# Optimization experiments

Measured on AMD Instinct MI355X. Metric: run time of the kernel, lower is better.

Reference implementation:

```python
import jax, jax.numpy as jnp
import numpy as np

HEADS = 4
OUT_CH = 16
NEG_SLOPE = 0.2


def setup_inputs() -> dict:
    key = jax.random.key(0)
    k1, k2, k3, k4 = jax.random.split(key, 4)
    N, E, IN = 50000, 800000, 128
    x = jax.random.normal(k1, (N, IN), dtype=jnp.float32)
    edge_index = jax.random.randint(k2, (2, E), 0, N, dtype=jnp.int32)
    weight = jax.random.normal(k3, (IN, HEADS * OUT_CH), dtype=jnp.float32) * 0.1
    att = jax.random.normal(k4, (1, HEADS, 2 * OUT_CH), dtype=jnp.float32) * 0.1
    bias = jnp.zeros((HEADS * OUT_CH,), dtype=jnp.float32)
    return {"x": x, "edge_index": edge_index, "weight": weight, "att": att, "bias": bias}


def reference(x, edge_index, weight, att, bias):
    N = x.shape[0]
    # add self loops
    loops = jnp.broadcast_to(jnp.arange(N, dtype=edge_index.dtype)[None, :], (2, N))
    ei = jnp.concatenate([edge_index, loops], axis=1)  # [2, E+N]
    h = (x @ weight).reshape(N, HEADS, OUT_CH)  # [N, H, C]
    row, col = ei[0], ei[1]
    x_i = h[row]  # [E', H, C]
    x_j = h[col]  # [E', H, C]
    att_i = att[:, :, :OUT_CH]  # [1, H, C]
    att_j = att[:, :, OUT_CH:]
    alpha = (x_i * att_i).sum(-1) + (x_j * att_j).sum(-1)  # [E', H]
    alpha = jax.nn.leaky_relu(alpha, NEG_SLOPE)
    # NOTE: faithful to the source, softmax over the heads dim (dim=1)
    alpha = jax.nn.softmax(alpha, axis=1)
    out = jnp.zeros((N, HEADS, OUT_CH), dtype=x.dtype)
    out = out.at[col].add(x_i * alpha[..., None])  # scatter-add over destination col
    out = out.reshape(N, HEADS * OUT_CH) + bias
    return out
```

## Files before the change

### kernel.cpp

```cpp
#include <hip/hip_runtime.h>

#define HEADS 4
#define OUT_CH 16
#define CCH 64
#define IN_CH 128
#define NEG_SLOPE 0.2f
#define CAP 48
#define CAPB 5120
#define TILE_A 2048
#define BSTRIDE 32

typedef unsigned int       uint32;
typedef unsigned short     u16;
typedef __attribute__((ext_vector_type(8))) short short8;
typedef __attribute__((ext_vector_type(4))) float f32x4;

__device__ __forceinline__ uint32 bf16_rne(float f) {
    uint32 u = __float_as_uint(f);
    return (u + 0x7fffu + ((u >> 16) & 1u)) >> 16;
}

__global__ __launch_bounds__(256) void k_pre(int* __restrict__ cur, int N,
                                             const float* __restrict__ x,
                                             const float* __restrict__ w,
                                             const float* __restrict__ att,
                                             u16* __restrict__ wTg,
                                             int* __restrict__ bcur, int NBUK,
                                             float* __restrict__ d_i,
                                             float* __restrict__ d_j,
                                             int ZB) {
    int t = threadIdx.x;
    int b = blockIdx.x;

    if (b < ZB) {
        int i = b * 256 + t;
        if (i < N) cur[i] = 0;
        return;
    }
    if (b == ZB) {
        int c = t & 63, half = t >> 6;
        #pragma unroll
        for (int kk = 0; kk < 32; ++kk) {
            int k = half * 32 + kk;
            wTg[c * 128 + k] = (u16)bf16_rne(w[k * CCH + c]);
        }
        for (int i = t; i < NBUK * BSTRIDE; i += 256) bcur[i] = 0;
        return;
    }

    __shared__ float wXf[8][132];
    for (int idx = t; idx < 1024; idx += 256) {
        int k = idx >> 3, j = idx & 7, h = j & 3;
        const float* ab = att + h * (2 * OUT_CH) + ((j >= 4) ? OUT_CH : 0);
        float s = 0.f;
        #pragma unroll
        for (int c = 0; c < 16; ++c)
            s = fmaf(w[k * CCH + h * OUT_CH + c], ab[c], s);
        wXf[j][k] = s;
    }
    __syncthreads();

    int r = (b - ZB - 1) * 32 + (t >> 3);
    int j = t & 7;
    if (r >= N) return;
    const float4* x4 = (const float4*)(x + (size_t)r * IN_CH);
    float s0 = 0.f, s1 = 0.f, s2 = 0.f, s3 = 0.f;
    #pragma unroll
    for (int k4 = 0; k4 < 32; ++k4) {
        float4 v = x4[k4];
        s0 = fmaf(v.x, wXf[j][k4 * 4 + 0], s0);
        s1 = fmaf(v.y, wXf[j][k4 * 4 + 1], s1);
        s2 = fmaf(v.z, wXf[j][k4 * 4 + 2], s2);
        s3 = fmaf(v.w, wXf[j][k4 * 4 + 3], s3);
    }
    float d = (s0 + s1) + (s2 + s3);
    if (j < 4) d_i[r * HEADS + j] = d;
    else       d_j[r * HEADS + (j - 4)] = d;
}

__global__ __launch_bounds__(256) void k_fat(const float* __restrict__ x,
                                             const u16* __restrict__ wTg,
                                             u16* __restrict__ h_bf,
                                             const int* __restrict__ rows,
                                             const int* __restrict__ cols,
                                             int* __restrict__ bcur,
                                             uint32* __restrict__ bucketbuf,
                                             int N, int E, int GB, int NBUK) {
    int t = threadIdx.x;

    if ((int)blockIdx.x < GB) {
        int lane = t & 63;
        int col = lane & 15, g = (lane >> 4) * 8;
        int tile = blockIdx.x * 4 + (t >> 6);
        int ntiles = (N + 15) >> 4;
        if (tile >= ntiles) return;

        int r0 = tile * 16 + (lane & 15);
        if (r0 >= N) r0 = N - 1;
        const float* xp = x + (size_t)r0 * IN_CH + g;
        float4 cu[8];
        #pragma unroll
        for (int kc = 0; kc < 4; ++kc) {
            cu[kc * 2]     = *(const float4*)(xp + kc * 32);
            cu[kc * 2 + 1] = *(const float4*)(xp + kc * 32 + 4);
        }

        short8 bfrag[4][4];
        #pragma unroll
        for (int nt = 0; nt < 4; ++nt)
            #pragma unroll
            for (int kc = 0; kc < 4; ++kc)
                bfrag[nt][kc] = *(const short8*)&wTg[(nt * 16 + col) * 128 + kc * 32 + g];

        short8 af[4];
        #pragma unroll
        for (int kc = 0; kc < 4; ++kc) {
            float4 u = cu[kc * 2], v = cu[kc * 2 + 1];
            short8 s;
            s[0] = (short)bf16_rne(u.x); s[1] = (short)bf16_rne(u.y);
            s[2] = (short)bf16_rne(u.z); s[3] = (short)bf16_rne(u.w);
            s[4] = (short)bf16_rne(v.x); s[5] = (short)bf16_rne(v.y);
            s[6] = (short)bf16_rne(v.z); s[7] = (short)bf16_rne(v.w);
            af[kc] = s;
        }

        f32x4 acc[4] = {{0.f,0.f,0.f,0.f},{0.f,0.f,0.f,0.f},
                        {0.f,0.f,0.f,0.f},{0.f,0.f,0.f,0.f}};
        #pragma unroll
        for (int kc = 0; kc < 4; ++kc)
            #pragma unroll
            for (int nt = 0; nt < 4; ++nt)
                acc[nt] = __builtin_amdgcn_mfma_f32_16x16x32_bf16(
                    af[kc], bfrag[nt][kc], acc[nt], 0, 0, 0);

        int rb = tile * 16;
        #pragma unroll
        for (int nt = 0; nt < 4; ++nt)
            #pragma unroll
            for (int r = 0; r < 4; ++r) {
                int row = rb + (lane >> 4) * 4 + r;
                if (row < N)
                    h_bf[(size_t)row * CCH + nt * 16 + col] =
                        (u16)bf16_rne(acc[nt][r]);
            }
    } else {
        __shared__ int lcnt[256];
        __shared__ int lofs[256];
        __shared__ int lbase[256];
        __shared__ int wsum[4];
        __shared__ uint32 recbuf[TILE_A];
        __shared__ int    gbuf[TILE_A];
        int b = (int)blockIdx.x - GB;
        int e0 = b * TILE_A;
        int tot = E + N;
        int lane = t & 63, wid = t >> 6;

        lcnt[t] = 0;
        __syncthreads();

        int mybkt[8], myrank[8];
        uint32 myrec[8];
        #pragma unroll
        for (int i = 0; i < 8; ++i) {
            int e = e0 + i * 256 + t;
            if (e < tot) {
                int c = (e < E) ? cols[e] : (e - E);
                int r = (e < E) ? rows[e] : c;
                int bk = c >> 8;
                mybkt[i] = bk;
                myrec[i] = (uint32)r | ((uint32)(c & 255) << 17);
                myrank[i] = atomicAdd(&lcnt[bk], 1);
            } else {
                mybkt[i] = -1;
            }
        }
        __syncthreads();

        int v = lcnt[t];
        int sc = v;
        #pragma unroll
        for (int off = 1; off < 64; off <<= 1) {
            int u = __shfl_up(sc, off);
            if (lane >= off) sc += u;
        }
        if (lane == 63) wsum[wid] = sc;
        __syncthreads();
        int wb = 0;
        for (int j = 0; j < wid; ++j) wb += wsum[j];
        lofs[t] = wb + sc - v;
        if (t < NBUK && v > 0)
            lbase[t] = atomicAdd(&bcur[t * BSTRIDE], v);
        __syncthreads();

        #pragma unroll
        for (int i = 0; i < 8; ++i) {
            if (mybkt[i] < 0) continue;
            int bk = mybkt[i];
            int slot = lofs[bk] + myrank[i];
            int bpos = lbase[bk] + myrank[i];
            recbuf[slot] = myrec[i];
            gbuf[slot] = (bpos < CAPB) ? (bk * CAPB + bpos) : -1;
        }
        __syncthreads();

        int nrec = tot - e0;
        if (nrec > TILE_A) nrec = TILE_A;
        for (int sidx = t; sidx < nrec; sidx += 256) {
            int gp = gbuf[sidx];
            if (gp >= 0) bucketbuf[gp] = recbuf[sidx];
        }
    }
}

__global__ __launch_bounds__(256) void k_bucket(const int* __restrict__ bcur,
                                                const uint32* __restrict__ bucketbuf,
                                                uint32* __restrict__ srec,
                                                int* __restrict__ cur, int N) {
    __shared__ uint32 win[256 * CAP];
    __shared__ int lcur[256];
    int t = threadIdx.x;
    int b = blockIdx.x;

    lcur[t] = 0;
    __syncthreads();

    int cnt = bcur[b * BSTRIDE];
    if (cnt > CAPB) cnt = CAPB;
    const uint32* bb = bucketbuf + (size_t)b * CAPB;
    for (int i = t; i < cnt; i += 256) {
        uint32 rec = bb[i];
        int crel = (rec >> 17) & 255;
        int pos = atomicAdd(&lcur[crel], 1);
        if (pos < CAP)
            win[crel * CAP + pos] = rec & 0x1FFFFu;
    }
    __syncthreads();

    int c0 = b << 8;
    int nd = N - c0;
    if (nd > 256) nd = 256;
    int nent = nd * CAP;
    uint32* dst = srec + (size_t)c0 * CAP;
    for (int i = t; i < nent; i += 256) dst[i] = win[i];
    if (t < nd) {
        int v = lcur[t];
        cur[c0 + t] = (v > CAP) ? CAP : v;
    }
}

__global__ __launch_bounds__(256) void k_accum(const int* __restrict__ cur,
                                               const uint32* __restrict__ srec,
                                               const u16* __restrict__ h_bf,
                                               const float* __restrict__ d_i,
                                               const float* __restrict__ d_j,
                                               const float* __restrict__ bias,
                                               float* __restrict__ out, int N) {
    int t = threadIdx.x;
    int wid = t >> 6, lane = t & 63;
    int g = lane >> 4, sub = lane & 15;
    int node = blockIdx.x * 16 + wid * 4 + g;
    int c = (node < N) ? node : N - 1;

    int dg = cur[c];
    if (dg > CAP) dg = CAP;
    int s = c * CAP;
    int md = dg;
    md = max(md, __shfl_xor(md, 16));
    md = max(md, __shfl_xor(md, 32));

    float4 dj4 = *(const float4*)(d_j + (size_t)c * HEADS);
    int hsel = sub >> 2;
    float a0 = 0.f, a1 = 0.f, a2 = 0.f, a3 = 0.f;

    #pragma unroll 4
    for (int r = 0; r < md; ++r) {
        int idx = s + ((r < dg) ? r : (dg - 1));
        int row = (int)srec[idx];
        float4 di4 = *(const float4*)(d_i + (size_t)row * HEADS);
        float l0 = di4.x + dj4.x, l1 = di4.y + dj4.y;
        float l2 = di4.z + dj4.z, l3 = di4.w + dj4.w;
        l0 = l0 > 0.f ? l0 : NEG_SLOPE * l0;
        l1 = l1 > 0.f ? l1 : NEG_SLOPE * l1;
        l2 = l2 > 0.f ? l2 : NEG_SLOPE * l2;
        l3 = l3 > 0.f ? l3 : NEG_SLOPE * l3;
        float m = fmaxf(fmaxf(l0, l1), fmaxf(l2, l3));
        float e0 = __expf(l0 - m), e1 = __expf(l1 - m);
        float e2 = __expf(l2 - m), e3 = __expf(l3 - m);
        float inv = 1.f / (e0 + e1 + e2 + e3);
        float eh = (hsel < 2) ? (hsel == 0 ? e0 : e1) : (hsel == 2 ? e2 : e3);
        float a = eh * inv;
        if (r >= dg) a = 0.f;
        uint2 hb = *(const uint2*)(h_bf + (size_t)row * CCH + sub * 4);
        a0 = fmaf(__uint_as_float(hb.x << 16),           a, a0);
        a1 = fmaf(__uint_as_float(hb.x & 0xffff0000u),   a, a1);
        a2 = fmaf(__uint_as_float(hb.y << 16),           a, a2);
        a3 = fmaf(__uint_as_float(hb.y & 0xffff0000u),   a, a3);
    }

    if (node < N) {
        float4 b = *(const float4*)(bias + sub * 4);
        float4 o = {a0 + b.x, a1 + b.y, a2 + b.z, a3 + b.w};
        *(float4*)(out + (size_t)node * CCH + sub * 4) = o;
    }
}

extern "C" void kernel_launch(void* const* d_in, const int* in_sizes, int n_in,
                              void* d_out, int out_size, void* d_ws, size_t ws_size,
                              hipStream_t stream) {
    const float* x    = (const float*)d_in[0];
    const int*   ei   = (const int*)  d_in[1];
    const float* w    = (const float*)d_in[2];
    const float* att  = (const float*)d_in[3];
    const float* bias = (const float*)d_in[4];
    float* out = (float*)d_out;

    int N = in_sizes[0] / IN_CH;
    int E = in_sizes[1] / 2;
    const int* rows = ei;
    const int* cols = ei + E;
    int total_e = E + N;
    int NBUK = (N + 255) >> 8;

    char* ws = (char*)d_ws;
    auto carve = [&](size_t bytes) {
        char* p = ws;
        ws += (bytes + 255) & ~(size_t)255;
        return p;
    };
    u16*    h_bf      = (u16*)   carve((size_t)N * CCH * 2);
    float*  di        = (float*) carve((size_t)N * HEADS * 4);
    float*  dj        = (float*) carve((size_t)N * HEADS * 4);
    int*    cur       = (int*)   carve((size_t)N * 4);
    int*    bcur      = (int*)   carve((size_t)NBUK * BSTRIDE * 4);
    uint32* srec      = (uint32*)carve((size_t)N * CAP * 4);
    u16*    wTg       = (u16*)   carve((size_t)64 * 128 * 2);
    uint32* bucketbuf = (uint32*)carve((size_t)NBUK * CAPB * 4);

    int ntiles = (N + 15) >> 4;
    int GB = (ntiles + 3) / 4;
    int AB = (total_e + TILE_A - 1) / TILE_A;
    int ZB = (N + 255) / 256;
    int DB = (N + 31) / 32;

    k_pre<<<ZB + 1 + DB, 256, 0, stream>>>(cur, N, x, w, att, wTg, bcur, NBUK,
                                           di, dj, ZB);
    k_fat<<<GB + AB, 256, 0, stream>>>(x, wTg, h_bf, rows, cols,
                                       bcur, bucketbuf, N, E, GB, NBUK);
    k_bucket<<<NBUK, 256, 0, stream>>>(bcur, bucketbuf, srec, cur, N);
    k_accum<<<(N + 15) / 16, 256, 0, stream>>>(cur, srec, h_bf, di, dj, bias, out, N);
}
```

Before: 97.97 us.

## Fuse attention logits into MFMA GEMM, precompute quantized softmax weights in bucketing

Computes the per-node attention logits d_i/d_j as an extra MFMA tile in the projection kernel, which removes the separate fp32 pass over x in k_pre. Softmax weights are now computed once per edge in k_bucket and packed as 11-bit quantized values next to the row index in 64-bit records. The accumulation is split into two launches, each over half of the channels, so each pass gathers a smaller h slice, and it uses nontemporal loads and stores. The cost is twice as much record storage and reading the records twice. The 11-bit weights and bf16 logit weights also reduce accuracy.

Measured after the change: 100.2 us. 1.02x slower.

```diff
diff --git a/kernel.cpp b/kernel.cpp
--- a/kernel.cpp
+++ b/kernel.cpp
@@ -11,76 +11,51 @@
 #define BSTRIDE 32
 
 typedef unsigned int       uint32;
+typedef unsigned long long u64;
 typedef unsigned short     u16;
 typedef __attribute__((ext_vector_type(8))) short short8;
 typedef __attribute__((ext_vector_type(4))) float f32x4;
+typedef __attribute__((ext_vector_type(2))) float f32x2;
 
 __device__ __forceinline__ uint32 bf16_rne(float f) {
     uint32 u = __float_as_uint(f);
     return (u + 0x7fffu + ((u >> 16) & 1u)) >> 16;
 }
 
-__global__ __launch_bounds__(256) void k_pre(int* __restrict__ cur, int N,
-                                             const float* __restrict__ x,
-                                             const float* __restrict__ w,
+__global__ __launch_bounds__(256) void k_pre(const float* __restrict__ w,
                                              const float* __restrict__ att,
                                              u16* __restrict__ wTg,
-                                             int* __restrict__ bcur, int NBUK,
+                                             u16* __restrict__ wXg,
+                                             int* __restrict__ bcur, int NBUK) {
+    int t = threadIdx.x;
+    int c = t & 63, half = t >> 6;
+    #pragma unroll
+    for (int kk = 0; kk < 32; ++kk) {
+        int k = half * 32 + kk;
+        wTg[c * 128 + k] = (u16)bf16_rne(w[k * CCH + c]);
+    }
+    int j = t & 7, h = j & 3, kb = t >> 3;
+    const float* ab = att + h * (2 * OUT_CH) + ((j >= 4) ? OUT_CH : 0);
+    #pragma unroll
+    for (int kk = 0; kk < 4; ++kk) {
+        int k = kb * 4 + kk;
+        float s = 0.f;
+        #pragma unroll
+        for (int cc = 0; cc < 16; ++cc)
+            s = fmaf(w[k * CCH + h * OUT_CH + cc], ab[cc], s);
+        wXg[j * 128 + k] = (u16)bf16_rne(s);
+    }
+    for (int i = t; i < 8 * 128; i += 256) wXg[8 * 128 + i] = 0;
+    for (int i = t; i < NBUK * BSTRIDE; i += 256) bcur[i] = 0;
+}
+
+__global__ __launch_bounds__(256) void k_fat(const float* __restrict__ x,
+                                             const u16* __restrict__ wTg,
+                                             const u16* __restrict__ wXg,
+                                             u16* __restrict__ h0,
+                                             u16* __restrict__ h1,
                                              float* __restrict__ d_i,
                                              float* __restrict__ d_j,
-                                             int ZB) {
-    int t = threadIdx.x;
-    int b = blockIdx.x;
-
-    if (b < ZB) {
-        int i = b * 256 + t;
-        if (i < N) cur[i] = 0;
-        return;
-    }
-    if (b == ZB) {
-        int c = t & 63, half = t >> 6;
-        #pragma unroll
-        for (int kk = 0; kk < 32; ++kk) {
-            int k = half * 32 + kk;
-            wTg[c * 128 + k] = (u16)bf16_rne(w[k * CCH + c]);
-        }
-        for (int i = t; i < NBUK * BSTRIDE; i += 256) bcur[i] = 0;
-        return;
-    }
-
-    __shared__ float wXf[8][132];
-    for (int idx = t; idx < 1024; idx += 256) {
-        int k = idx >> 3, j = idx & 7, h = j & 3;
-        const float* ab = att + h * (2 * OUT_CH) + ((j >= 4) ? OUT_CH : 0);
-        float s = 0.f;
-        #pragma unroll
-        for (int c = 0; c < 16; ++c)
-            s = fmaf(w[k * CCH + h * OUT_CH + c], ab[c], s);
-        wXf[j][k] = s;
-    }
-    __syncthreads();
-
-    int r = (b - ZB - 1) * 32 + (t >> 3);
-    int j = t & 7;
-    if (r >= N) return;
-    const float4* x4 = (const float4*)(x + (size_t)r * IN_CH);
-    float s0 = 0.f, s1 = 0.f, s2 = 0.f, s3 = 0.f;
-    #pragma unroll
-    for (int k4 = 0; k4 < 32; ++k4) {
-        float4 v = x4[k4];
-        s0 = fmaf(v.x, wXf[j][k4 * 4 + 0], s0);
-        s1 = fmaf(v.y, wXf[j][k4 * 4 + 1], s1);
-        s2 = fmaf(v.z, wXf[j][k4 * 4 + 2], s2);
-        s3 = fmaf(v.w, wXf[j][k4 * 4 + 3], s3);
-    }
-    float d = (s0 + s1) + (s2 + s3);
-    if (j < 4) d_i[r * HEADS + j] = d;
-    else       d_j[r * HEADS + (j - 4)] = d;
-}
-
-__global__ __launch_bounds__(256) void k_fat(const float* __restrict__ x,
-                                             const u16* __restrict__ wTg,
-                                             u16* __restrict__ h_bf,
                                              const int* __restrict__ rows,
                                              const int* __restrict__ cols,
                                              int* __restrict__ bcur,
@@ -105,12 +80,15 @@
             cu[kc * 2 + 1] = *(const float4*)(xp + kc * 32 + 4);
         }
 
-        short8 bfrag[4][4];
+        short8 bfrag[4][4], bfrag5[4];
         #pragma unroll
         for (int nt = 0; nt < 4; ++nt)
             #pragma unroll
             for (int kc = 0; kc < 4; ++kc)
                 bfrag[nt][kc] = *(const short8*)&wTg[(nt * 16 + col) * 128 + kc * 32 + g];
+        #pragma unroll
+        for (int kc = 0; kc < 4; ++kc)
+            bfrag5[kc] = *(const short8*)&wXg[col * 128 + kc * 32 + g];
 
         short8 af[4];
         #pragma unroll
@@ -126,23 +104,39 @@
 
         f32x4 acc[4] = {{0.f,0.f,0.f,0.f},{0.f,0.f,0.f,0.f},
                         {0.f,0.f,0.f,0.f},{0.f,0.f,0.f,0.f}};
-        #pragma unroll
-        for (int kc = 0; kc < 4; ++kc)
+        f32x4 accX = {0.f, 0.f, 0.f, 0.f};
+        #pragma unroll
+        for (int kc = 0; kc < 4; ++kc) {
             #pragma unroll
             for (int nt = 0; nt < 4; ++nt)
                 acc[nt] = __builtin_amdgcn_mfma_f32_16x16x32_bf16(
                     af[kc], bfrag[nt][kc], acc[nt], 0, 0, 0);
+            accX = __builtin_amdgcn_mfma_f32_16x16x32_bf16(
+                af[kc], bfrag5[kc], accX, 0, 0, 0);
+        }
 
         int rb = tile * 16;
         #pragma unroll
-        for (int nt = 0; nt < 4; ++nt)
+        for (int nt = 0; nt < 4; ++nt) {
+            u16* hp = (nt < 2) ? h0 : h1;
+            int cc = (nt & 1) * 16 + col;
             #pragma unroll
             for (int r = 0; r < 4; ++r) {
                 int row = rb + (lane >> 4) * 4 + r;
                 if (row < N)
-                    h_bf[(size_t)row * CCH + nt * 16 + col] =
-                        (u16)bf16_rne(acc[nt][r]);
+                    hp[(size_t)row * 32 + cc] = (u16)bf16_rne(acc[nt][r]);
             }
+        }
+        if (col < 8) {
+            #pragma unroll
+            for (int r = 0; r < 4; ++r) {
+                int row = rb + (lane >> 4) * 4 + r;
+                if (row < N) {
+                    if (col < 4) d_i[row * HEADS + col] = accX[r];
+                    else         d_j[row * HEADS + (col - 4)] = accX[r];
+                }
+            }
+        }
     } else {
         __shared__ int lcnt[256];
         __shared__ int lofs[256];
@@ -214,14 +208,21 @@
 
 __global__ __launch_bounds__(256) void k_bucket(const int* __restrict__ bcur,
                                                 const uint32* __restrict__ bucketbuf,
-                                                uint32* __restrict__ srec,
+                                                const float* __restrict__ d_i,
+                                                const float* __restrict__ d_j,
+                                                u64* __restrict__ srec,
                                                 int* __restrict__ cur, int N) {
-    __shared__ uint32 win[256 * CAP];
+    __shared__ u64 win[256 * CAP];
     __shared__ int lcur[256];
+    __shared__ float4 djl[256];
     int t = threadIdx.x;
     int b = blockIdx.x;
+    int c0 = b << 8;
 
     lcur[t] = 0;
+    int cidx = c0 + t;
+    djl[t] = (cidx < N) ? *(const float4*)(d_j + (size_t)cidx * HEADS)
+                        : make_float4(0.f, 0.f, 0.f, 0.f);
     __syncthreads();
 
     int cnt = bcur[b * BSTRIDE];
@@ -229,54 +230,10 @@
     const uint32* bb = bucketbuf + (size_t)b * CAPB;
     for (int i = t; i < cnt; i += 256) {
         uint32 rec = bb[i];
+        int row  = rec & 0x1FFFF;
         int crel = (rec >> 17) & 255;
-        int pos = atomicAdd(&lcur[crel], 1);
-        if (pos < CAP)
-            win[crel * CAP + pos] = rec & 0x1FFFFu;
-    }
-    __syncthreads();
-
-    int c0 = b << 8;
-    int nd = N - c0;
-    if (nd > 256) nd = 256;
-    int nent = nd * CAP;
-    uint32* dst = srec + (size_t)c0 * CAP;
-    for (int i = t; i < nent; i += 256) dst[i] = win[i];
-    if (t < nd) {
-        int v = lcur[t];
-        cur[c0 + t] = (v > CAP) ? CAP : v;
-    }
-}
-
-__global__ __launch_bounds__(256) void k_accum(const int* __restrict__ cur,
-                                               const uint32* __restrict__ srec,
-                                               const u16* __restrict__ h_bf,
-                                               const float* __restrict__ d_i,
-                                               const float* __restrict__ d_j,
-                                               const float* __restrict__ bias,
-                                               float* __restrict__ out, int N) {
-    int t = threadIdx.x;
-    int wid = t >> 6, lane = t & 63;
-    int g = lane >> 4, sub = lane & 15;
-    int node = blockIdx.x * 16 + wid * 4 + g;
-    int c = (node < N) ? node : N - 1;
-
-    int dg = cur[c];
-    if (dg > CAP) dg = CAP;
-    int s = c * CAP;
-    int md = dg;
-    md = max(md, __shfl_xor(md, 16));
-    md = max(md, __shfl_xor(md, 32));
-
-    float4 dj4 = *(const float4*)(d_j + (size_t)c * HEADS);
-    int hsel = sub >> 2;
-    float a0 = 0.f, a1 = 0.f, a2 = 0.f, a3 = 0.f;
-
-    #pragma unroll 4
-    for (int r = 0; r < md; ++r) {
-        int idx = s + ((r < dg) ? r : (dg - 1));
-        int row = (int)srec[idx];
         float4 di4 = *(const float4*)(d_i + (size_t)row * HEADS);
+        float4 dj4 = djl[crel];
         float l0 = di4.x + dj4.x, l1 = di4.y + dj4.y;
         float l2 = di4.z + dj4.z, l3 = di4.w + dj4.w;
         l0 = l0 > 0.f ? l0 : NEG_SLOPE * l0;
@@ -287,20 +244,70 @@
         float e0 = __expf(l0 - m), e1 = __expf(l1 - m);
         float e2 = __expf(l2 - m), e3 = __expf(l3 - m);
         float inv = 1.f / (e0 + e1 + e2 + e3);
-        float eh = (hsel < 2) ? (hsel == 0 ? e0 : e1) : (hsel == 2 ? e2 : e3);
-        float a = eh * inv;
+        uint32 q0 = (uint32)(e0 * inv * 2047.f + 0.5f);
+        uint32 q1 = (uint32)(e1 * inv * 2047.f + 0.5f);
+        uint32 q2 = (uint32)(e2 * inv * 2047.f + 0.5f);
+        uint32 q3 = (uint32)(e3 * inv * 2047.f + 0.5f);
+        u64 prec = (u64)(uint32)row
+                 | ((u64)q0 << 17) | ((u64)q1 << 28)
+                 | ((u64)q2 << 39) | ((u64)q3 << 50);
+        int pos = atomicAdd(&lcur[crel], 1);
+        if (pos < CAP)
+            win[crel * CAP + pos] = prec;
+    }
+    __syncthreads();
+
+    int nd = N - c0;
+    if (nd > 256) nd = 256;
+    int nent = nd * CAP;
+    u64* dst = srec + (size_t)c0 * CAP;
+    for (int i = t; i < nent; i += 256) dst[i] = win[i];
+    if (t < nd) {
+        int v = lcur[t];
+        cur[c0 + t] = (v > CAP) ? CAP : v;
+    }
+}
+
+__global__ __launch_bounds__(256) void k_accum(const int* __restrict__ cur,
+                                               const u64* __restrict__ srec,
+                                               const u16* __restrict__ hp,
+                                               const float* __restrict__ bias,
+                                               float* __restrict__ out,
+                                               int N, int half) {
+    int t = threadIdx.x;
+    int wid = t >> 6, lane = t & 63;
+    int g = lane >> 4, sub = lane & 15;
+    int node = blockIdx.x * 16 + wid * 4 + g;
+    int c = (node < N) ? node : N - 1;
+
+    int dg = cur[c];
+    if (dg > CAP) dg = CAP;
+    size_t s = (size_t)c * CAP;
+    int md = dg;
+    md = max(md, __shfl_xor(md, 16));
+    md = max(md, __shfl_xor(md, 32));
+
+    int ch0 = half * 32 + sub * 2;
+    int shift = 17 + 11 * (ch0 >> 4);
+    float a0 = 0.f, a1 = 0.f;
+
+    #pragma unroll 8
+    for (int r = 0; r < md; ++r) {
+        size_t idx = s + ((r < dg) ? r : (dg - 1));
+        u64 rec = __builtin_nontemporal_load(srec + idx);
+        int row = (int)((uint32)rec & 0x1FFFFu);
+        float a = (float)((uint32)(rec >> shift) & 0x7FFu) * (1.f / 2047.f);
         if (r >= dg) a = 0.f;
-        uint2 hb = *(const uint2*)(h_bf + (size_t)row * CCH + sub * 4);
-        a0 = fmaf(__uint_as_float(hb.x << 16),           a, a0);
-        a1 = fmaf(__uint_as_float(hb.x & 0xffff0000u),   a, a1);
-        a2 = fmaf(__uint_as_float(hb.y << 16),           a, a2);
-        a3 = fmaf(__uint_as_float(hb.y & 0xffff0000u),   a, a3);
+        uint32 hb = *(const uint32*)(hp + (size_t)row * 32 + sub * 2);
+        a0 = fmaf(__uint_as_float(hb << 16),         a, a0);
+        a1 = fmaf(__uint_as_float(hb & 0xffff0000u), a, a1);
     }
 
     if (node < N) {
-        float4 b = *(const float4*)(bias + sub * 4);
-        float4 o = {a0 + b.x, a1 + b.y, a2 + b.z, a3 + b.w};
-        *(float4*)(out + (size_t)node * CCH + sub * 4) = o;
+        f32x2 o;
+        o.x = a0 + bias[ch0];
+        o.y = a1 + bias[ch0 + 1];
+        __builtin_nontemporal_store(o, (f32x2*)(out + (size_t)node * CCH + ch0));
     }
 }
 
@@ -327,25 +334,26 @@
         ws += (bytes + 255) & ~(size_t)255;
         return p;
     };
-    u16*    h_bf      = (u16*)   carve((size_t)N * CCH * 2);
+    u16*    h0        = (u16*)   carve((size_t)N * 32 * 2);
+    u16*    h1        = (u16*)   carve((size_t)N * 32 * 2);
     float*  di        = (float*) carve((size_t)N * HEADS * 4);
     float*  dj        = (float*) carve((size_t)N * HEADS * 4);
     int*    cur       = (int*)   carve((size_t)N * 4);
     int*    bcur      = (int*)   carve((size_t)NBUK * BSTRIDE * 4);
-    uint32* srec      = (uint32*)carve((size_t)N * CAP * 4);
+    u64*    srec      = (u64*)   carve((size_t)N * CAP * 8);
     u16*    wTg       = (u16*)   carve((size_t)64 * 128 * 2);
+    u16*    wXg       = (u16*)   carve((size_t)16 * 128 * 2);
     uint32* bucketbuf = (uint32*)carve((size_t)NBUK * CAPB * 4);
 
     int ntiles = (N + 15) >> 4;
     int GB = (ntiles + 3) / 4;
     int AB = (total_e + TILE_A - 1) / TILE_A;
-    int ZB = (N + 255) / 256;
-    int DB = (N + 31) / 32;
-
-    k_pre<<<ZB + 1 + DB, 256, 0, stream>>>(cur, N, x, w, att, wTg, bcur, NBUK,
-                                           di, dj, ZB);
-    k_fat<<<GB + AB, 256, 0, stream>>>(x, wTg, h_bf, rows, cols,
+    int NACC = (N + 15) / 16;
+
+    k_pre<<<1, 256, 0, stream>>>(w, att, wTg, wXg, bcur, NBUK);
+    k_fat<<<GB + AB, 256, 0, stream>>>(x, wTg, wXg, h0, h1, di, dj, rows, cols,
                                        bcur, bucketbuf, N, E, GB, NBUK);
-    k_bucket<<<NBUK, 256, 0, stream>>>(bcur, bucketbuf, srec, cur, N);
-    k_accum<<<(N + 15) / 16, 256, 0, stream>>>(cur, srec, h_bf, di, dj, bias, out, N);
-}
+    k_bucket<<<NBUK, 256, 0, stream>>>(bcur, bucketbuf, di, dj, srec, cur, N);
+    k_accum<<<NACC, 256, 0, stream>>>(cur, srec, h0, bias, out, N, 0);
+    k_accum<<<NACC, 256, 0, stream>>>(cur, srec, h1, bias, out, N, 1);
+}
```
